# Performance work log

Measured on AMD Instinct MI355X. Metric: run time of the kernel, lower is better.

Reference implementation:

```python
import jax, jax.numpy as jnp
import numpy as np

N_NODES = 100000
N_EDGES = 3200000
IN_DIM, HD_DIM, OUT_DIM = 512, 256, 128


def spmm(edge_row, edge_col, edge_val, x):
    # y[i] = sum_{e: row[e]=i} val[e] * x[col[e]]  -- sparse adj @ dense x
    msgs = edge_val[:, None] * x[edge_col]          # [E, D]
    return jax.ops.segment_sum(msgs, edge_row, num_segments=N_NODES)


def setup_inputs() -> dict:
    key = jax.random.key(0)
    k1, k2, k3, k4, k5, k6, k7, k8 = jax.random.split(key, 8)
    x = jax.random.normal(k1, (N_NODES, IN_DIM), dtype=jnp.float32)
    edge_row = jax.random.randint(k2, (N_EDGES,), 0, N_NODES, dtype=jnp.int64)
    edge_col = jax.random.randint(k3, (N_EDGES,), 0, N_NODES, dtype=jnp.int64)
    edge_val = jax.random.uniform(k4, (N_EDGES,), dtype=jnp.float32)
    s0 = 1.0 / np.sqrt(IN_DIM)
    s1 = 1.0 / np.sqrt(HD_DIM)
    W0 = jax.random.uniform(k5, (IN_DIM, HD_DIM), dtype=jnp.float32, minval=-s0, maxval=s0)
    b0 = jax.random.uniform(k6, (HD_DIM,), dtype=jnp.float32, minval=-s0, maxval=s0)
    W1 = jax.random.uniform(k7, (HD_DIM, OUT_DIM), dtype=jnp.float32, minval=-s1, maxval=s1)
    b1 = jax.random.uniform(k8, (OUT_DIM,), dtype=jnp.float32, minval=-s1, maxval=s1)
    return {"x": x, "edge_row": edge_row, "edge_col": edge_col, "edge_val": edge_val,
            "W0": W0, "b0": b0, "W1": W1, "b1": b1}


def reference(x, edge_row, edge_col, edge_val, W0, b0, W1, b1):
    # eval mode: dropout is identity
    h = x @ W0 + b0                                  # li0: [N, HD]
    h = spmm(edge_row, edge_col, edge_val, h)        # adj @ h
    h = spmm(edge_row, edge_col, edge_val, h)        # adj @ (adj @ h)
    return jax.nn.relu(h) @ W1 + b1                  # li1(relu(.)): [N, OUT]
```

## Files before the change

kernel.cpp:

```cpp
#include <hip/hip_runtime.h>

#define N_NODES 100000
#define N_EDGES 3200000
#define IN_DIM  512
#define HD_DIM  256
#define OUT_DIM 128

#define NBINS  391
#define BINCAP 9216
#define EPT    16
#define EPB    (256 * EPT)

typedef short   short8  __attribute__((ext_vector_type(8)));
typedef unsigned short ushort8 __attribute__((ext_vector_type(8)));
typedef float   floatx4 __attribute__((ext_vector_type(4)));

__device__ __forceinline__ unsigned short f2bf(float f) {
    unsigned int u = __float_as_uint(f);
    u += 0x7fffu + ((u >> 16) & 1u);
    return (unsigned short)(u >> 16);
}

__device__ __forceinline__ unsigned f2bf_pk(float lo, float hi) {
    unsigned r;
    asm("v_cvt_pk_bf16_f32 %0, %1, %2" : "=v"(r) : "v"(lo), "v"(hi));
    return r;
}


__global__ __launch_bounds__(256) void bin_scatter(const int* __restrict__ erow,
                                                   const int* __restrict__ ecol,
                                                   const float* __restrict__ eval,
                                                   int* __restrict__ gcnt,
                                                   uint2* __restrict__ binned, int E) {
    __shared__ int hist[NBINS];
    __shared__ int sd[512];
    __shared__ int lbase[NBINS];
    __shared__ int gbase[NBINS];
    __shared__ int cur[NBINS];
    __shared__ unsigned short sbin[EPB];
    __shared__ uint2 sedge[EPB];

    const int t = threadIdx.x;
    for (int i = t; i < NBINS; i += 256) hist[i] = 0;
    __syncthreads();

    long base = (long)blockIdx.x * EPB + t * EPT;
    int rows[EPT];
    const bool valid = base < E;
    if (valid) {
        const int4* p = (const int4*)(erow + base);
#pragma unroll
        for (int v = 0; v < 4; v++) {
            int4 r = p[v];
            rows[4 * v + 0] = r.x; rows[4 * v + 1] = r.y;
            rows[4 * v + 2] = r.z; rows[4 * v + 3] = r.w;
        }
#pragma unroll
        for (int u = 0; u < EPT; u++) atomicAdd(&hist[rows[u] >> 8], 1);
    }
    __syncthreads();

    sd[t]       = (t < NBINS) ? hist[t] : 0;
    sd[t + 256] = (t + 256 < NBINS) ? hist[t + 256] : 0;
    __syncthreads();
    for (int off = 1; off < 512; off <<= 1) {
        int a0 = (t >= off) ? sd[t - off] : 0;
        int a1 = (t + 256 >= off) ? sd[t + 256 - off] : 0;
        __syncthreads();
        sd[t] += a0;
        sd[t + 256] += a1;
        __syncthreads();
    }

    for (int i = t; i < NBINS; i += 256) {
        int h  = hist[i];
        int lb = sd[i] - h;
        lbase[i] = lb;
        cur[i]   = lb;
        gbase[i] = h ? (i * BINCAP + atomicAdd(&gcnt[i], h)) : 0;
    }
    __syncthreads();

    if (valid) {
        const int4*   pc = (const int4*)(ecol + base);
        const float4* pv = (const float4*)(eval + base);
#pragma unroll
        for (int v = 0; v < 4; v++) {
            int4 c4 = pc[v];
            float4 v4 = pv[v];
            int   cs[4] = {c4.x, c4.y, c4.z, c4.w};
            float vs[4] = {v4.x, v4.y, v4.z, v4.w};
#pragma unroll
            for (int u = 0; u < 4; u++) {
                int r = rows[4 * v + u];
                int bin = r >> 8;
                int lpos = atomicAdd(&cur[bin], 1);
                sedge[lpos] = make_uint2(((unsigned)(r & 255) << 20) | (unsigned)cs[u],
                                         __float_as_uint(vs[u]));
                sbin[lpos] = (unsigned short)bin;
            }
        }
    }
    __syncthreads();

    const int ns = sd[NBINS - 1];
    for (int i = t; i < ns; i += 256) {
        int bin = sbin[i];
        int gpos = gbase[bin] + (i - lbase[bin]);
        if (gpos < (bin + 1) * BINCAP)
            binned[gpos] = sedge[i];
    }
}

__global__ __launch_bounds__(256) void bin_finalize(const int* __restrict__ gcnt,
                                                    const uint2* __restrict__ binned,
                                                    int* __restrict__ rowptr,
                                                    int* __restrict__ binend,
                                                    uint2* __restrict__ csr) {
    __shared__ int hist[256];
    __shared__ int cur[256];
    __shared__ uint2 stage[BINCAP];
    const int b = blockIdx.x;
    const int t = threadIdx.x;
    int n = gcnt[b];
    if (n > BINCAP) n = BINCAP;
    const int s = b * BINCAP;

    hist[t] = 0;
    __syncthreads();
    for (int i = s + t; i < s + n; i += 256)
        atomicAdd(&hist[binned[i].x >> 20], 1);
    __syncthreads();
    int v = hist[t];
    for (int off = 1; off < 256; off <<= 1) {
        int add = (t >= off) ? hist[t - off] : 0;
        __syncthreads();
        hist[t] += add;
        __syncthreads();
    }
    int excl = hist[t] - v;
    int r = (b << 8) + t;
    if (r <= N_NODES) rowptr[r] = s + excl;
    if (t == 0) binend[b] = s + n;
    cur[t] = excl;
    __syncthreads();
    for (int i = s + t; i < s + n; i += 256) {
        uint2 ev = binned[i];
        int pos = atomicAdd(&cur[ev.x >> 20], 1);
        stage[pos] = make_uint2(ev.x & 0xFFFFFu, ev.y);
    }
    __syncthreads();
    for (int i = t; i < n; i += 256)
        csr[s + i] = stage[i];
}


__global__ void transpose_bf16(const float* __restrict__ in, unsigned short* __restrict__ out,
                               int K, int N) {
    int idx = blockIdx.x * blockDim.x + threadIdx.x;
    if (idx < K * N) {
        int k = idx / N, n = idx - k * N;
        out[n * K + k] = f2bf(in[idx]);
    }
}


template <bool A_FP32, bool RELU_A, bool OUT_BF16, int BN>
__global__ __launch_bounds__(256, 2) void gemm_mfma(const void* __restrict__ Av,
                                                    const unsigned short* __restrict__ BT,
                                                    const float* __restrict__ bias,
                                                    void* __restrict__ Cv,
                                                    int M, int N, int K) {
    constexpr int NJ = BN / 32;
    __shared__ unsigned short As[128 * 40];
    __shared__ unsigned short Bs[BN * 40];
    const int tid  = threadIdx.x;
    const int lane = tid & 63;
    const int wv   = tid >> 6;
    const int wm   = (wv >> 1) * 64;
    const int wn   = (wv & 1) * (BN / 2);
    const int mrow = lane & 15;
    const int q    = lane >> 4;
    const int bm   = blockIdx.x * 128;
    const int bn   = blockIdx.y * BN;

    floatx4 acc[4][NJ] = {};

    const int srow = tid >> 1;
    const int skh  = (tid & 1) * 16;

    for (int k0 = 0; k0 < K; k0 += 32) {
        {
            const int grow = bm + srow;
            if (A_FP32) {
                uint4 w0, w1;
                if (grow < M) {
                    const float* A = (const float*)Av;
                    const float4* p = (const float4*)&A[(long)grow * K + k0 + skh];
                    float4 f;
                    f = p[0]; w0.x = f2bf_pk(f.x, f.y); w0.y = f2bf_pk(f.z, f.w);
                    f = p[1]; w0.z = f2bf_pk(f.x, f.y); w0.w = f2bf_pk(f.z, f.w);
                    f = p[2]; w1.x = f2bf_pk(f.x, f.y); w1.y = f2bf_pk(f.z, f.w);
                    f = p[3]; w1.z = f2bf_pk(f.x, f.y); w1.w = f2bf_pk(f.z, f.w);
                } else {
                    w0 = make_uint4(0, 0, 0, 0);
                    w1 = make_uint4(0, 0, 0, 0);
                }
                *(uint4*)&As[srow * 40 + skh]     = w0;
                *(uint4*)&As[srow * 40 + skh + 8] = w1;
            } else {
                unsigned short tmp[16];
                const unsigned short* A = (const unsigned short*)Av;
                if (grow < M) {
                    const ushort8* p = (const ushort8*)&A[(long)grow * K + k0 + skh];
                    ushort8 u0 = p[0], u1 = p[1];
#pragma unroll
                    for (int v = 0; v < 8; v++) { tmp[v] = u0[v]; tmp[8 + v] = u1[v]; }
                    if (RELU_A) {
#pragma unroll
                        for (int v = 0; v < 16; v++)
                            if (tmp[v] & 0x8000u) tmp[v] = 0;
                    }
                } else {
#pragma unroll
                    for (int v = 0; v < 16; v++) tmp[v] = 0;
                }
                ushort8* dst = (ushort8*)&As[srow * 40 + skh];
                ushort8 w0, w1;
#pragma unroll
                for (int v = 0; v < 8; v++) { w0[v] = tmp[v]; w1[v] = tmp[8 + v]; }
                dst[0] = w0;
                dst[1] = w1;
            }
        }
        if (BN == 128) {
            const int gn = bn + srow;
            const ushort8* p = (const ushort8*)&BT[(long)gn * K + k0 + skh];
            ushort8* dst = (ushort8*)&Bs[srow * 40 + skh];
            dst[0] = p[0];
            dst[1] = p[1];
        } else {
            const int gn = bn + tid;
            const ushort8* p = (const ushort8*)&BT[(long)gn * K + k0];
            ushort8* dst = (ushort8*)&Bs[tid * 40];
            dst[0] = p[0];
            dst[1] = p[1];
            dst[2] = p[2];
            dst[3] = p[3];
        }
        __syncthreads();

        short8 af[4], bf[NJ];
#pragma unroll
        for (int i = 0; i < 4; i++)
            af[i] = *(const short8*)&As[(wm + i * 16 + mrow) * 40 + q * 8];
#pragma unroll
        for (int j = 0; j < NJ; j++)
            bf[j] = *(const short8*)&Bs[(wn + j * 16 + mrow) * 40 + q * 8];
#pragma unroll
        for (int i = 0; i < 4; i++)
#pragma unroll
            for (int j = 0; j < NJ; j++)
                acc[i][j] = __builtin_amdgcn_mfma_f32_16x16x32_bf16(af[i], bf[j], acc[i][j], 0, 0, 0);
        __syncthreads();
    }

#pragma unroll
    for (int i = 0; i < 4; i++) {
#pragma unroll
        for (int r = 0; r < 4; r++) {
            const int row = bm + wm + i * 16 + q * 4 + r;
            if (row < M) {
#pragma unroll
                for (int j = 0; j < NJ; j++) {
                    const int col = bn + wn + j * 16 + mrow;
                    float v = acc[i][j][r] + bias[col];
                    if (OUT_BF16)
                        ((unsigned short*)Cv)[(long)row * N + col] = f2bf(v);
                    else
                        ((float*)Cv)[(long)row * N + col] = v;
                }
            }
        }
    }
}


__global__ __launch_bounds__(256) void spmm_bf16(const int* __restrict__ rowptr,
                                                 const int* __restrict__ binend,
                                                 const uint2* __restrict__ edges,
                                                 const unsigned short* __restrict__ Hin,
                                                 unsigned short* __restrict__ Hout) {
    const int wave = threadIdx.x >> 6;
    const int lane = threadIdx.x & 63;
    const int r = blockIdx.x * 4 + wave;
    if (r >= N_NODES) return;
    const int s = rowptr[r];
    const int e = ((r & 255) == 255) ? binend[r >> 8] : rowptr[r + 1];
    const uint2* __restrict__ Hv = (const uint2*)Hin;
    float a0 = 0.f, a1 = 0.f, a2 = 0.f, a3 = 0.f;

    for (int base = s; base < e; base += 64) {
        int idx = base + lane;
        uint2 ev = (idx < e) ? edges[idx] : make_uint2(0u, 0u);
        int cnt = e - base;
        if (cnt > 64) cnt = 64;
        for (int j0 = 0; j0 < cnt; j0 += 8) {
            uint2 h[8];
            float v[8];
#pragma unroll
            for (int u = 0; u < 8; u++) {
                int   c = __shfl((int)ev.x, j0 + u);
                v[u]    = __uint_as_float((unsigned)__shfl((int)ev.y, j0 + u));
                h[u]    = Hv[((unsigned)c << 6) + lane];
            }
#pragma unroll
            for (int u = 0; u < 8; u++) {
                a0 += v[u] * __uint_as_float(h[u].x << 16);
                a1 += v[u] * __uint_as_float(h[u].x & 0xffff0000u);
                a2 += v[u] * __uint_as_float(h[u].y << 16);
                a3 += v[u] * __uint_as_float(h[u].y & 0xffff0000u);
            }
        }
    }
    uint2 o;
    o.x = (unsigned)f2bf(a0) | ((unsigned)f2bf(a1) << 16);
    o.y = (unsigned)f2bf(a2) | ((unsigned)f2bf(a3) << 16);
    ((uint2*)Hout)[((unsigned)r << 6) + lane] = o;
}


extern "C" void kernel_launch(void* const* d_in, const int* in_sizes, int n_in,
                              void* d_out, int out_size, void* d_ws, size_t ws_size,
                              hipStream_t stream) {
    const float* x    = (const float*)d_in[0];
    const int*   erow = (const int*)d_in[1];
    const int*   ecol = (const int*)d_in[2];
    const float* eval = (const float*)d_in[3];
    const float* W0   = (const float*)d_in[4];
    const float* b0   = (const float*)d_in[5];
    const float* W1   = (const float*)d_in[6];
    const float* b1   = (const float*)d_in[7];
    float* out = (float*)d_out;

    char* ws = (char*)d_ws;
    size_t off = 0;
    auto alloc = [&](size_t bytes) {
        void* p = ws + off;
        off += (bytes + 255) & ~(size_t)255;
        return p;
    };
    int*            rowptr   = (int*)alloc((N_NODES + 1) * sizeof(int));
    int*            gcnt     = (int*)alloc(NBINS * sizeof(int));
    int*            binend   = (int*)alloc(NBINS * sizeof(int));
    uint2*          binned   = (uint2*)alloc((size_t)NBINS * BINCAP * sizeof(uint2));
    uint2*          csr      = (uint2*)alloc((size_t)NBINS * BINCAP * sizeof(uint2));
    unsigned short* W0T      = (unsigned short*)alloc((size_t)IN_DIM * HD_DIM * sizeof(unsigned short));
    unsigned short* W1T      = (unsigned short*)alloc((size_t)HD_DIM * OUT_DIM * sizeof(unsigned short));
    unsigned short* Ha       = (unsigned short*)alloc((size_t)N_NODES * HD_DIM * sizeof(unsigned short));
    unsigned short* Hb       = (unsigned short*)alloc((size_t)N_NODES * HD_DIM * sizeof(unsigned short));

    const int nblk = (N_EDGES + EPB - 1) / EPB;

    hipMemsetAsync(gcnt, 0, NBINS * sizeof(int), stream);
    bin_scatter<<<nblk, 256, 0, stream>>>(erow, ecol, eval, gcnt, binned, N_EDGES);
    bin_finalize<<<NBINS, 256, 0, stream>>>(gcnt, binned, rowptr, binend, csr);

    transpose_bf16<<<(IN_DIM * HD_DIM + 255) / 256, 256, 0, stream>>>(W0, W0T, IN_DIM, HD_DIM);
    transpose_bf16<<<(HD_DIM * OUT_DIM + 255) / 256, 256, 0, stream>>>(W1, W1T, HD_DIM, OUT_DIM);

    gemm_mfma<true, false, true, 256><<<dim3((N_NODES + 127) / 128, HD_DIM / 256), 256, 0, stream>>>(
        x, W0T, b0, Ha, N_NODES, HD_DIM, IN_DIM);

    spmm_bf16<<<(N_NODES + 3) / 4, 256, 0, stream>>>(rowptr, binend, csr, Ha, Hb);
    spmm_bf16<<<(N_NODES + 3) / 4, 256, 0, stream>>>(rowptr, binend, csr, Hb, Ha);

    gemm_mfma<false, true, false, 128><<<dim3((N_NODES + 127) / 128, OUT_DIM / 128), 256, 0, stream>>>(
        Ha, W1T, b1, out, N_NODES, OUT_DIM, HD_DIM);
}
```

Before: 861.8 us.

## Fuse per-bin CSR sort into first SpMM and shrink bins to 64 rows

Bins are made finer (64 rows each instead of 256), and the scatter kernel now writes edges straight to global memory through per-bin atomics, with no LDS staging or prefix scan. The finalize/sort pass is merged into the first SpMM: each block sorts its bin in LDS, writes the CSR for the second SpMM, and computes its 64 output rows from the LDS-sorted edges. This removes a separate sort kernel and a round trip through global memory. The two weight transposes become one launch, and nontemporal loads and stores are added in the SpMM. In exchange, the scatter writes to global memory are less coalesced, and a bin holding more than 2560 edges would be silently truncated.

New measurement: 894.6 us. 1.04x slower.

```diff
diff --git a/kernel.cpp b/kernel.cpp
--- a/kernel.cpp
+++ b/kernel.cpp
@@ -6,8 +6,9 @@
 #define HD_DIM  256
 #define OUT_DIM 128
 
-#define NBINS  391
-#define BINCAP 9216
+#define NBINS  1563
+#define BINCAP 2560
+#define SORT_IT 10
 #define EPT    16
 #define EPB    (256 * EPT)
 
@@ -34,13 +35,8 @@
                                                    int* __restrict__ gcnt,
                                                    uint2* __restrict__ binned, int E) {
     __shared__ int hist[NBINS];
-    __shared__ int sd[512];
-    __shared__ int lbase[NBINS];
+    __shared__ int cur[NBINS];
     __shared__ int gbase[NBINS];
-    __shared__ int cur[NBINS];
-    __shared__ unsigned short sbin[EPB];
-    __shared__ uint2 sedge[EPB];
-
     const int t = threadIdx.x;
     for (int i = t; i < NBINS; i += 256) hist[i] = 0;
     __syncthreads();
@@ -57,27 +53,13 @@
             rows[4 * v + 2] = r.z; rows[4 * v + 3] = r.w;
         }
 #pragma unroll
-        for (int u = 0; u < EPT; u++) atomicAdd(&hist[rows[u] >> 8], 1);
-    }
-    __syncthreads();
-
-    sd[t]       = (t < NBINS) ? hist[t] : 0;
-    sd[t + 256] = (t + 256 < NBINS) ? hist[t + 256] : 0;
-    __syncthreads();
-    for (int off = 1; off < 512; off <<= 1) {
-        int a0 = (t >= off) ? sd[t - off] : 0;
-        int a1 = (t + 256 >= off) ? sd[t + 256 - off] : 0;
-        __syncthreads();
-        sd[t] += a0;
-        sd[t + 256] += a1;
-        __syncthreads();
-    }
+        for (int u = 0; u < EPT; u++) atomicAdd(&hist[rows[u] >> 6], 1);
+    }
+    __syncthreads();
 
     for (int i = t; i < NBINS; i += 256) {
-        int h  = hist[i];
-        int lb = sd[i] - h;
-        lbase[i] = lb;
-        cur[i]   = lb;
+        int h = hist[i];
+        cur[i] = 0;
         gbase[i] = h ? (i * BINCAP + atomicAdd(&gcnt[i], h)) : 0;
     }
     __syncthreads();
@@ -94,74 +76,133 @@
 #pragma unroll
             for (int u = 0; u < 4; u++) {
                 int r = rows[4 * v + u];
-                int bin = r >> 8;
-                int lpos = atomicAdd(&cur[bin], 1);
-                sedge[lpos] = make_uint2(((unsigned)(r & 255) << 20) | (unsigned)cs[u],
-                                         __float_as_uint(vs[u]));
-                sbin[lpos] = (unsigned short)bin;
-            }
-        }
-    }
-    __syncthreads();
-
-    const int ns = sd[NBINS - 1];
-    for (int i = t; i < ns; i += 256) {
-        int bin = sbin[i];
-        int gpos = gbase[bin] + (i - lbase[bin]);
-        if (gpos < (bin + 1) * BINCAP)
-            binned[gpos] = sedge[i];
-    }
-}
-
-__global__ __launch_bounds__(256) void bin_finalize(const int* __restrict__ gcnt,
-                                                    const uint2* __restrict__ binned,
-                                                    int* __restrict__ rowptr,
-                                                    int* __restrict__ binend,
-                                                    uint2* __restrict__ csr) {
-    __shared__ int hist[256];
-    __shared__ int cur[256];
-    __shared__ uint2 stage[BINCAP];
+                int bin = r >> 6;
+                int lofs = atomicAdd(&cur[bin], 1);
+                binned[gbase[bin] + lofs] =
+                    make_uint2(((unsigned)(r & 63) << 26) | (unsigned)cs[u],
+                               __float_as_uint(vs[u]));
+            }
+        }
+    }
+}
+
+
+__global__ __launch_bounds__(256) void spmm_sort(const int* __restrict__ gcnt,
+                                                 const uint2* __restrict__ binned,
+                                                 int* __restrict__ rowptr,
+                                                 int* __restrict__ binend,
+                                                 uint2* __restrict__ csr,
+                                                 const unsigned short* __restrict__ Hin,
+                                                 unsigned short* __restrict__ Hout) {
+    __shared__ uint2 ssort[BINCAP];
+    __shared__ int hist[64];
+    __shared__ int sd[64];
+    __shared__ int cur[64];
+    const int t = threadIdx.x;
     const int b = blockIdx.x;
-    const int t = threadIdx.x;
     int n = gcnt[b];
     if (n > BINCAP) n = BINCAP;
     const int s = b * BINCAP;
-
-    hist[t] = 0;
-    __syncthreads();
-    for (int i = s + t; i < s + n; i += 256)
-        atomicAdd(&hist[binned[i].x >> 20], 1);
-    __syncthreads();
-    int v = hist[t];
-    for (int off = 1; off < 256; off <<= 1) {
-        int add = (t >= off) ? hist[t - off] : 0;
+    const int rows_base = b << 6;
+
+    if (t < 64) hist[t] = 0;
+    __syncthreads();
+
+    uint2 ereg[SORT_IT];
+#pragma unroll
+    for (int it = 0; it < SORT_IT; it++) {
+        int i = it * 256 + t;
+        if (i < n) {
+            ereg[it] = binned[s + i];
+            atomicAdd(&hist[ereg[it].x >> 26], 1);
+        }
+    }
+    __syncthreads();
+
+    if (t < 64) sd[t] = hist[t];
+    __syncthreads();
+#pragma unroll
+    for (int off = 1; off < 64; off <<= 1) {
+        int add = 0;
+        if (t < 64 && t >= off) add = sd[t - off];
         __syncthreads();
-        hist[t] += add;
+        if (t < 64) sd[t] += add;
         __syncthreads();
     }
-    int excl = hist[t] - v;
-    int r = (b << 8) + t;
-    if (r <= N_NODES) rowptr[r] = s + excl;
+    if (t < 64) {
+        int ex = sd[t] - hist[t];
+        cur[t] = ex;
+        int r = rows_base + t;
+        if (r <= N_NODES) rowptr[r] = s + ex;
+    }
     if (t == 0) binend[b] = s + n;
-    cur[t] = excl;
-    __syncthreads();
-    for (int i = s + t; i < s + n; i += 256) {
-        uint2 ev = binned[i];
-        int pos = atomicAdd(&cur[ev.x >> 20], 1);
-        stage[pos] = make_uint2(ev.x & 0xFFFFFu, ev.y);
-    }
-    __syncthreads();
-    for (int i = t; i < n; i += 256)
-        csr[s + i] = stage[i];
-}
-
-
-__global__ void transpose_bf16(const float* __restrict__ in, unsigned short* __restrict__ out,
-                               int K, int N) {
+    __syncthreads();
+
+#pragma unroll
+    for (int it = 0; it < SORT_IT; it++) {
+        int i = it * 256 + t;
+        if (i < n) {
+            int rl = ereg[it].x >> 26;
+            int p = atomicAdd(&cur[rl], 1);
+            ssort[p] = make_uint2(ereg[it].x & 0x03FFFFFFu, ereg[it].y);
+        }
+    }
+    __syncthreads();
+
+    for (int i = t; i < n; i += 256) csr[s + i] = ssort[i];
+
+    const int wave = t >> 6;
+    const int lane = t & 63;
+    const uint2* __restrict__ Hv = (const uint2*)Hin;
+    for (int rl = wave; rl < 64; rl += 4) {
+        const int r = rows_base + rl;
+        if (r >= N_NODES) break;
+        const int ks = sd[rl] - hist[rl];
+        const int ke = sd[rl];
+        float a0 = 0.f, a1 = 0.f, a2 = 0.f, a3 = 0.f;
+        for (int j0 = ks; j0 < ke; j0 += 8) {
+            int m = ke - j0;
+            if (m > 8) m = 8;
+            unsigned c[8];
+            float    v[8];
+            uint2    h[8];
+#pragma unroll
+            for (int u = 0; u < 8; u++) {
+                if (u < m) {
+                    uint2 e = ssort[j0 + u];
+                    c[u] = e.x;
+                    v[u] = __uint_as_float(e.y);
+                } else { c[u] = 0u; v[u] = 0.f; }
+            }
+#pragma unroll
+            for (int u = 0; u < 8; u++) h[u] = Hv[(c[u] << 6) + lane];
+#pragma unroll
+            for (int u = 0; u < 8; u++) {
+                a0 += v[u] * __uint_as_float(h[u].x << 16);
+                a1 += v[u] * __uint_as_float(h[u].x & 0xffff0000u);
+                a2 += v[u] * __uint_as_float(h[u].y << 16);
+                a3 += v[u] * __uint_as_float(h[u].y & 0xffff0000u);
+            }
+        }
+        unsigned long long o = (unsigned long long)((unsigned)f2bf(a0) | ((unsigned)f2bf(a1) << 16))
+                             | ((unsigned long long)((unsigned)f2bf(a2) | ((unsigned)f2bf(a3) << 16)) << 32);
+        __builtin_nontemporal_store(o, (unsigned long long*)Hout + (((unsigned)r << 6) + lane));
+    }
+}
+
+
+__global__ void transpose_w(const float* __restrict__ W0, unsigned short* __restrict__ W0T,
+                            const float* __restrict__ W1, unsigned short* __restrict__ W1T) {
     int idx = blockIdx.x * blockDim.x + threadIdx.x;
-    if (idx < K * N) {
-        int k = idx / N, n = idx - k * N;
-        out[n * K + k] = f2bf(in[idx]);
+    if (idx < IN_DIM * HD_DIM) {
+        int k = idx / HD_DIM, n = idx - k * HD_DIM;
+        W0T[n * IN_DIM + k] = f2bf(W0[idx]);
+    } else {
+        int j = idx - IN_DIM * HD_DIM;
+        if (j < HD_DIM * OUT_DIM) {
+            int k = j / OUT_DIM, n = j - k * OUT_DIM;
+            W1T[n * HD_DIM + k] = f2bf(W1[j]);
+        }
     }
 }
 
@@ -297,13 +338,19 @@
     const int r = blockIdx.x * 4 + wave;
     if (r >= N_NODES) return;
     const int s = rowptr[r];
-    const int e = ((r & 255) == 255) ? binend[r >> 8] : rowptr[r + 1];
+    const int e = ((r & 63) == 63) ? binend[r >> 6] : rowptr[r + 1];
     const uint2* __restrict__ Hv = (const uint2*)Hin;
     float a0 = 0.f, a1 = 0.f, a2 = 0.f, a3 = 0.f;
 
     for (int base = s; base < e; base += 64) {
         int idx = base + lane;
-        uint2 ev = (idx < e) ? edges[idx] : make_uint2(0u, 0u);
+        uint2 ev = make_uint2(0u, 0u);
+        if (idx < e) {
+            unsigned long long raw =
+                __builtin_nontemporal_load((const unsigned long long*)edges + idx);
+            ev.x = (unsigned)raw;
+            ev.y = (unsigned)(raw >> 32);
+        }
         int cnt = e - base;
         if (cnt > 64) cnt = 64;
         for (int j0 = 0; j0 < cnt; j0 += 8) {
@@ -324,10 +371,9 @@
             }
         }
     }
-    uint2 o;
-    o.x = (unsigned)f2bf(a0) | ((unsigned)f2bf(a1) << 16);
-    o.y = (unsigned)f2bf(a2) | ((unsigned)f2bf(a3) << 16);
-    ((uint2*)Hout)[((unsigned)r << 6) + lane] = o;
+    unsigned long long o = (unsigned long long)((unsigned)f2bf(a0) | ((unsigned)f2bf(a1) << 16))
+                         | ((unsigned long long)((unsigned)f2bf(a2) | ((unsigned)f2bf(a3) << 16)) << 32);
+    __builtin_nontemporal_store(o, (unsigned long long*)Hout + (((unsigned)r << 6) + lane));
 }
 
 
@@ -365,15 +411,15 @@
 
     hipMemsetAsync(gcnt, 0, NBINS * sizeof(int), stream);
     bin_scatter<<<nblk, 256, 0, stream>>>(erow, ecol, eval, gcnt, binned, N_EDGES);
-    bin_finalize<<<NBINS, 256, 0, stream>>>(gcnt, binned, rowptr, binend, csr);
-
-    transpose_bf16<<<(IN_DIM * HD_DIM + 255) / 256, 256, 0, stream>>>(W0, W0T, IN_DIM, HD_DIM);
-    transpose_bf16<<<(HD_DIM * OUT_DIM + 255) / 256, 256, 0, stream>>>(W1, W1T, HD_DIM, OUT_DIM);
+
+    transpose_w<<<(IN_DIM * HD_DIM + HD_DIM * OUT_DIM + 255) / 256, 256, 0, stream>>>(
+        W0, W0T, W1, W1T);
 
     gemm_mfma<true, false, true, 256><<<dim3((N_NODES + 127) / 128, HD_DIM / 256), 256, 0, stream>>>(
         x, W0T, b0, Ha, N_NODES, HD_DIM, IN_DIM);
 
-    spmm_bf16<<<(N_NODES + 3) / 4, 256, 0, stream>>>(rowptr, binend, csr, Ha, Hb);
+    spmm_sort<<<NBINS, 256, 0, stream>>>(gcnt, binned, rowptr, binend, csr, Ha, Hb);
+
     spmm_bf16<<<(N_NODES + 3) / 4, 256, 0, stream>>>(rowptr, binend, csr, Hb, Ha);
 
     gemm_mfma<false, true, false, 128><<<dim3((N_NODES + 127) / 128, OUT_DIM / 128), 256, 0, stream>>>(
```
